# Kernel tuning notes

Hardware: AMD Instinct MI355X
Metric: run time of the kernel (lower is better)

The kernel has to match this reference:

```python
import jax, jax.numpy as jnp
import numpy as np

N = 500000      # num_edges
D = 128         # embedding_dim
S = 256         # num_samples (negatives)
TEMPERATURE = 0.1
EPS_NORM = 1e-12  # torch F.normalize eps
EPS_COS = 1e-8    # torch F.cosine_similarity eps


def setup_inputs() -> dict:
    key = jax.random.key(0)
    k1, k2, k3 = jax.random.split(key, 3)
    edge_embeddings = jax.random.normal(k1, (N, D), dtype=jnp.float32)
    positive_indices = jax.random.randint(k2, (N,), 0, N, dtype=jnp.int64)
    negative_indices = jax.random.randint(k3, (S,), 0, N, dtype=jnp.int64)
    return {
        "edge_embeddings": edge_embeddings,
        "positive_indices": positive_indices,
        "negative_indices": negative_indices,
    }


def _l2_normalize(x, eps):
    # matches torch: x / max(||x||_2, eps)
    n = jnp.sqrt(jnp.sum(x * x, axis=-1, keepdims=True))
    return x / jnp.maximum(n, eps)


def reference(edge_embeddings, positive_indices, negative_indices):
    # Normalize once; positives reuse the same per-row normalization.
    norm_all = _l2_normalize(edge_embeddings, EPS_NORM)          # [N, D]
    pos_norm = norm_all[positive_indices]                         # [N, D]
    positive_sim = jnp.sum(norm_all * pos_norm, axis=-1)          # [N]

    # cosine_similarity uses eps=1e-8 denominator clamp
    norm_all_cos = _l2_normalize(edge_embeddings, EPS_COS)        # [N, D]
    neg_norm = norm_all_cos[negative_indices]                     # [S, D]
    negative_sim = jnp.einsum('nd,sd->ns', norm_all_cos, neg_norm)  # [N, S]

    positive_logit = positive_sim / TEMPERATURE                   # [N]
    negative_logit = negative_sim / TEMPERATURE                   # [N, S]
    negative = jax.nn.logsumexp(negative_logit, axis=1) - jnp.log(jnp.float32(S))
    loss = -jnp.mean(positive_logit - negative)
    return loss
```

## Files before the change

kernel.cpp:

```cpp
#include <hip/hip_runtime.h>
#include <hip/hip_bf16.h>
#include <math.h>

#define D 128
#define S 256
#define ROWS 64
#define LOG_S 5.545177444479562f

typedef __attribute__((ext_vector_type(8)))  short    short8;
typedef __attribute__((ext_vector_type(8)))  __bf16   bf16x8;
typedef __attribute__((ext_vector_type(16))) float    floatx16;

typedef const __attribute__((address_space(1))) void gas_void;
typedef __attribute__((address_space(3))) void las_void;

__device__ __forceinline__ unsigned short f2bf(float x) {
  __hip_bfloat16 h = __float2bfloat16(x);
  return *(unsigned short*)&h;
}

__global__ void neg_norm_kernel(const float* __restrict__ emb,
                                const int* __restrict__ negidx,
                                unsigned short* __restrict__ negsw) {
  int s = blockIdx.x;
  int L = threadIdx.x;
  long idx = (long)negidx[s];
  float2 v = *(const float2*)(emb + idx * D + L * 2);
  float ss = v.x * v.x + v.y * v.y;
#pragma unroll
  for (int off = 1; off < 64; off <<= 1) ss += __shfl_xor(ss, off);
  float sc = 10.0f / fmaxf(sqrtf(ss), 1e-8f);
  int chunk = s >> 7, nr = s & 127;
  int lu = L >> 2, pos = (L & 3) * 2;
  int u = lu ^ (nr & 15);
  ushort2 o = make_ushort2(f2bf(v.x * sc), f2bf(v.y * sc));
  *(ushort2*)(negsw + chunk * 16384 + nr * 128 + u * 8 + pos) = o;
}

__global__ __launch_bounds__(256, 3)
void hyper_main(const float* __restrict__ emb,
                const int* __restrict__ posidx,
                const unsigned short* __restrict__ negsw,
                double* __restrict__ acc,
                int N) {
  __shared__ __align__(16) char smem[49152];
  unsigned short* rows_l = (unsigned short*)smem;
  unsigned short* negs_l = (unsigned short*)(smem + 16384);

  const int t = threadIdx.x;
  const int lane = t & 63;
  const int w = t >> 6;
  const long rbase = (long)blockIdx.x * ROWS;

  {
    const char* g = (const char*)negsw + w * 8192 + lane * 16;
    char* l = (char*)negs_l + w * 8192;
#pragma unroll
    for (int i = 0; i < 8; ++i)
      __builtin_amdgcn_global_load_lds((gas_void*)(g + i * 1024),
                                       (las_void*)(l + i * 1024), 16, 0, 0);
  }

  const int r  = t >> 2;
  const int qq = t & 3;
  long n = rbase + r;
  bool valid = (n < (long)N);
  long pi = 0;
  if (valid) pi = (long)posidx[n];

  float4 v[8];
  float ssv = 0.f, ssp = 0.f, dp = 0.f;
#pragma unroll
  for (int k = 0; k < 8; ++k) {
    int c4 = qq + 4 * k;
    float4 vv = make_float4(0.f, 0.f, 0.f, 0.f);
    float4 pp = make_float4(0.f, 0.f, 0.f, 0.f);
    if (valid) {
      vv = *(const float4*)(emb + n * D + c4 * 4);
      pp = *(const float4*)(emb + pi * D + c4 * 4);
    }
    v[k] = vv;
    ssv += vv.x*vv.x + vv.y*vv.y + vv.z*vv.z + vv.w*vv.w;
    ssp += pp.x*pp.x + pp.y*pp.y + pp.z*pp.z + pp.w*pp.w;
    dp  += vv.x*pp.x + vv.y*pp.y + vv.z*pp.z + vv.w*pp.w;
  }
#pragma unroll
  for (int off = 1; off < 4; off <<= 1) {
    ssv += __shfl_xor(ssv, off);
    ssp += __shfl_xor(ssp, off);
    dp  += __shfl_xor(dp,  off);
  }
  float inv8 = 1.0f / fmaxf(sqrtf(ssv), 1e-8f);
#pragma unroll
  for (int k = 0; k < 8; ++k) {
    int c4 = qq + 4 * k;
    int u = (c4 >> 1) ^ (r & 15);
    ushort4 o = make_ushort4(f2bf(v[k].x*inv8), f2bf(v[k].y*inv8),
                             f2bf(v[k].z*inv8), f2bf(v[k].w*inv8));
    *(ushort4*)&rows_l[r * 128 + u * 8 + (c4 & 1) * 4] = o;
  }
  float possum = 0.f;
  if (qq == 0 && valid) {
    float invv = 1.0f / fmaxf(sqrtf(ssv), 1e-12f);
    float invp = 1.0f / fmaxf(sqrtf(ssp), 1e-12f);
    possum = dp * invv * invp * 10.0f;
  }

  const int q   = lane >> 5;
  const int ln  = lane & 31;
  const int tr  = w >> 1;
  const int chh = w & 1;
  const int arow  = tr * 32 + ln;
  const int nrow0 = chh * 64 + ln;
  const int nrow1 = nrow0 + 32;

  float se[16];
#pragma unroll
  for (int i = 0; i < 16; ++i) se[i] = 0.f;

  for (int c = 0; c < 2; ++c) {
    __syncthreads();
    floatx16 acc0 = {};
    floatx16 acc1 = {};
#pragma unroll
    for (int ki = 0; ki < 8; ++ki) {
      int lu = ki * 2 + q;
      short8 a  = *(const short8*)&rows_l[arow  * 128 + (lu ^ (arow  & 15)) * 8];
      short8 b0 = *(const short8*)&negs_l[nrow0 * 128 + (lu ^ (nrow0 & 15)) * 8];
      short8 b1 = *(const short8*)&negs_l[nrow1 * 128 + (lu ^ (nrow1 & 15)) * 8];
      acc0 = __builtin_amdgcn_mfma_f32_32x32x16_bf16(
          __builtin_bit_cast(bf16x8, a), __builtin_bit_cast(bf16x8, b0), acc0, 0, 0, 0);
      acc1 = __builtin_amdgcn_mfma_f32_32x32x16_bf16(
          __builtin_bit_cast(bf16x8, a), __builtin_bit_cast(bf16x8, b1), acc1, 0, 0, 0);
    }
    if (c == 0) {
      __syncthreads();
      const char* g = (const char*)negsw + 32768 + w * 8192 + lane * 16;
      char* l = (char*)negs_l + w * 8192;
#pragma unroll
      for (int i = 0; i < 8; ++i)
        __builtin_amdgcn_global_load_lds((gas_void*)(g + i * 1024),
                                         (las_void*)(l + i * 1024), 16, 0, 0);
    }
#pragma unroll
    for (int rg = 0; rg < 16; ++rg)
      se[rg] += __expf(acc0[rg]) + __expf(acc1[rg]);
  }

#pragma unroll
  for (int rg = 0; rg < 16; ++rg) {
    float sv = se[rg];
#pragma unroll
    for (int off = 1; off < 32; off <<= 1) sv += __shfl_xor(sv, off);
    se[rg] = sv;
  }

  __syncthreads();
  float* sebuf = (float*)smem;
  if (ln == 0) {
#pragma unroll
    for (int rg = 0; rg < 16; ++rg) {
      int rr = tr * 32 + (rg & 3) + 8 * (rg >> 2) + 4 * q;
      sebuf[rr * 2 + chh] = se[rg];
    }
  }
  __syncthreads();

  float negterm = 0.f;
  if (t < 64) {
    long n2 = rbase + t;
    if (n2 < (long)N)
      negterm = __logf(sebuf[t * 2] + sebuf[t * 2 + 1]) - LOG_S;
  }

  float local = negterm - possum;
#pragma unroll
  for (int off = 1; off < 64; off <<= 1) local += __shfl_xor(local, off);
  float* red = (float*)(smem + 2048);
  if (lane == 0) red[w] = local;
  __syncthreads();
  if (t == 0) {
    double tot = (double)red[0] + (double)red[1] +
                 (double)red[2] + (double)red[3];
    atomicAdd(acc, tot);
  }
}

__global__ void finish_kernel(const double* __restrict__ acc,
                              float* __restrict__ out, int N) {
  out[0] = (float)(acc[0] / (double)N);
}

extern "C" void kernel_launch(void* const* d_in, const int* in_sizes, int n_in,
                              void* d_out, int out_size, void* d_ws, size_t ws_size,
                              hipStream_t stream) {
  const float* emb  = (const float*)d_in[0];
  const int* posidx = (const int*)d_in[1];
  const int* negidx = (const int*)d_in[2];
  int N = in_sizes[1];

  double* acc = (double*)d_ws;
  unsigned short* negsw = (unsigned short*)((char*)d_ws + 256);

  hipMemsetAsync(d_ws, 0, 256, stream);
  neg_norm_kernel<<<S, 64, 0, stream>>>(emb, negidx, negsw);
  int grid = (N + ROWS - 1) / ROWS;
  hyper_main<<<grid, 256, 0, stream>>>(emb, posidx, negsw, acc, N);
  finish_kernel<<<1, 1, 0, stream>>>(acc, (float*)d_out, N);
}
```

Before: 411.8 us.

## Keep A fragments in registers, double-buffer negative chunks, and use exp2 scaling

Each wave now owns 32 rows and converts its embeddings straight into MFMA A-fragments held in registers, with no round trip through LDS. The 256 negatives are streamed in four 64-row chunks through two LDS buffers so the next chunk loads while the current one is computed. Rows per block double to 128 and LDS drops to 32KB, allowing 4 blocks per CU. The logit scale folds in log2(e) so the exponential becomes a native exp2, and the cross-wave LDS reduction of per-row sums is removed. In exchange, register pressure rises from holding all A-fragments, and each row now runs more MFMA work per block.

```diff
diff --git a/kernel.cpp b/kernel.cpp
--- a/kernel.cpp
+++ b/kernel.cpp
@@ -4,8 +4,9 @@
 
 #define D 128
 #define S 256
-#define ROWS 64
+#define ROWS 128
 #define LOG_S 5.545177444479562f
+#define SCALE_EXP2 14.42695040888963f
 
 typedef __attribute__((ext_vector_type(8)))  short    short8;
 typedef __attribute__((ext_vector_type(8)))  __bf16   bf16x8;
@@ -14,9 +15,19 @@
 typedef const __attribute__((address_space(1))) void gas_void;
 typedef __attribute__((address_space(3))) void las_void;
 
+#if __has_builtin(__builtin_amdgcn_exp2f)
+#define EXP2(x) __builtin_amdgcn_exp2f(x)
+#else
+#define EXP2(x) exp2f(x)
+#endif
+
 __device__ __forceinline__ unsigned short f2bf(float x) {
   __hip_bfloat16 h = __float2bfloat16(x);
   return *(unsigned short*)&h;
+}
+
+__device__ __forceinline__ float dot4(float4 a, float4 b) {
+  return a.x*b.x + a.y*b.y + a.z*b.z + a.w*b.w;
 }
 
 __global__ void neg_norm_kernel(const float* __restrict__ emb,
@@ -29,122 +40,117 @@
   float ss = v.x * v.x + v.y * v.y;
 #pragma unroll
   for (int off = 1; off < 64; off <<= 1) ss += __shfl_xor(ss, off);
-  float sc = 10.0f / fmaxf(sqrtf(ss), 1e-8f);
-  int chunk = s >> 7, nr = s & 127;
+  float sc = SCALE_EXP2 / fmaxf(sqrtf(ss), 1e-8f);
+  int chunk = s >> 6, nr = s & 63;
   int lu = L >> 2, pos = (L & 3) * 2;
   int u = lu ^ (nr & 15);
   ushort2 o = make_ushort2(f2bf(v.x * sc), f2bf(v.y * sc));
-  *(ushort2*)(negsw + chunk * 16384 + nr * 128 + u * 8 + pos) = o;
-}
-
-__global__ __launch_bounds__(256, 3)
+  *(ushort2*)(negsw + chunk * 8192 + nr * 128 + u * 8 + pos) = o;
+}
+
+__global__ __launch_bounds__(256, 4)
 void hyper_main(const float* __restrict__ emb,
                 const int* __restrict__ posidx,
                 const unsigned short* __restrict__ negsw,
                 double* __restrict__ acc,
                 int N) {
-  __shared__ __align__(16) char smem[49152];
-  unsigned short* rows_l = (unsigned short*)smem;
-  unsigned short* negs_l = (unsigned short*)(smem + 16384);
+  __shared__ __align__(16) char smem[32768];
 
   const int t = threadIdx.x;
   const int lane = t & 63;
   const int w = t >> 6;
+  const int q = lane >> 5;
+  const int ln = lane & 31;
   const long rbase = (long)blockIdx.x * ROWS;
 
   {
-    const char* g = (const char*)negsw + w * 8192 + lane * 16;
-    char* l = (char*)negs_l + w * 8192;
-#pragma unroll
-    for (int i = 0; i < 8; ++i)
+    const char* g = (const char*)negsw + w * 4096 + lane * 16;
+    char* l = smem + w * 4096;
+#pragma unroll
+    for (int i = 0; i < 4; ++i)
       __builtin_amdgcn_global_load_lds((gas_void*)(g + i * 1024),
                                        (las_void*)(l + i * 1024), 16, 0, 0);
   }
 
-  const int r  = t >> 2;
-  const int qq = t & 3;
-  long n = rbase + r;
-  bool valid = (n < (long)N);
+  const long n = rbase + w * 32 + ln;
+  const bool valid = (n < (long)N);
   long pi = 0;
   if (valid) pi = (long)posidx[n];
 
-  float4 v[8];
+  float4 rv[8][2];
   float ssv = 0.f, ssp = 0.f, dp = 0.f;
 #pragma unroll
-  for (int k = 0; k < 8; ++k) {
-    int c4 = qq + 4 * k;
-    float4 vv = make_float4(0.f, 0.f, 0.f, 0.f);
-    float4 pp = make_float4(0.f, 0.f, 0.f, 0.f);
+  for (int ki = 0; ki < 8; ++ki) {
+    int off = (2 * ki + q) * 8;
+    float4 a0 = make_float4(0.f,0.f,0.f,0.f), a1 = a0, p0 = a0, p1 = a0;
     if (valid) {
-      vv = *(const float4*)(emb + n * D + c4 * 4);
-      pp = *(const float4*)(emb + pi * D + c4 * 4);
-    }
-    v[k] = vv;
-    ssv += vv.x*vv.x + vv.y*vv.y + vv.z*vv.z + vv.w*vv.w;
-    ssp += pp.x*pp.x + pp.y*pp.y + pp.z*pp.z + pp.w*pp.w;
-    dp  += vv.x*pp.x + vv.y*pp.y + vv.z*pp.z + vv.w*pp.w;
-  }
-#pragma unroll
-  for (int off = 1; off < 4; off <<= 1) {
-    ssv += __shfl_xor(ssv, off);
-    ssp += __shfl_xor(ssp, off);
-    dp  += __shfl_xor(dp,  off);
-  }
+      a0 = *(const float4*)(emb + n * D + off);
+      a1 = *(const float4*)(emb + n * D + off + 4);
+      p0 = *(const float4*)(emb + pi * D + off);
+      p1 = *(const float4*)(emb + pi * D + off + 4);
+    }
+    rv[ki][0] = a0; rv[ki][1] = a1;
+    ssv += dot4(a0, a0) + dot4(a1, a1);
+    ssp += dot4(p0, p0) + dot4(p1, p1);
+    dp  += dot4(a0, p0) + dot4(a1, p1);
+  }
+  ssv += __shfl_xor(ssv, 32);
+  ssp += __shfl_xor(ssp, 32);
+  dp  += __shfl_xor(dp,  32);
+
   float inv8 = 1.0f / fmaxf(sqrtf(ssv), 1e-8f);
-#pragma unroll
-  for (int k = 0; k < 8; ++k) {
-    int c4 = qq + 4 * k;
-    int u = (c4 >> 1) ^ (r & 15);
-    ushort4 o = make_ushort4(f2bf(v[k].x*inv8), f2bf(v[k].y*inv8),
-                             f2bf(v[k].z*inv8), f2bf(v[k].w*inv8));
-    *(ushort4*)&rows_l[r * 128 + u * 8 + (c4 & 1) * 4] = o;
-  }
+  short8 afrag[8];
+#pragma unroll
+  for (int ki = 0; ki < 8; ++ki) {
+    float4 a0 = rv[ki][0], a1 = rv[ki][1];
+    short8 t8;
+    t8[0] = (short)f2bf(a0.x * inv8); t8[1] = (short)f2bf(a0.y * inv8);
+    t8[2] = (short)f2bf(a0.z * inv8); t8[3] = (short)f2bf(a0.w * inv8);
+    t8[4] = (short)f2bf(a1.x * inv8); t8[5] = (short)f2bf(a1.y * inv8);
+    t8[6] = (short)f2bf(a1.z * inv8); t8[7] = (short)f2bf(a1.w * inv8);
+    afrag[ki] = t8;
+  }
+
   float possum = 0.f;
-  if (qq == 0 && valid) {
+  if (q == 0 && valid) {
     float invv = 1.0f / fmaxf(sqrtf(ssv), 1e-12f);
     float invp = 1.0f / fmaxf(sqrtf(ssp), 1e-12f);
     possum = dp * invv * invp * 10.0f;
   }
 
-  const int q   = lane >> 5;
-  const int ln  = lane & 31;
-  const int tr  = w >> 1;
-  const int chh = w & 1;
-  const int arow  = tr * 32 + ln;
-  const int nrow0 = chh * 64 + ln;
-  const int nrow1 = nrow0 + 32;
-
   float se[16];
 #pragma unroll
   for (int i = 0; i < 16; ++i) se[i] = 0.f;
 
-  for (int c = 0; c < 2; ++c) {
+  const int ulocal = (ln & 15);
+  for (int c = 0; c < 4; ++c) {
     __syncthreads();
+    if (c < 3) {
+      const char* g = (const char*)negsw + (c + 1) * 16384 + w * 4096 + lane * 16;
+      char* l = smem + ((c + 1) & 1) * 16384 + w * 4096;
+#pragma unroll
+      for (int i = 0; i < 4; ++i)
+        __builtin_amdgcn_global_load_lds((gas_void*)(g + i * 1024),
+                                         (las_void*)(l + i * 1024), 16, 0, 0);
+    }
+    const unsigned short* buf = (const unsigned short*)(smem + (c & 1) * 16384);
+
     floatx16 acc0 = {};
     floatx16 acc1 = {};
 #pragma unroll
     for (int ki = 0; ki < 8; ++ki) {
-      int lu = ki * 2 + q;
-      short8 a  = *(const short8*)&rows_l[arow  * 128 + (lu ^ (arow  & 15)) * 8];
-      short8 b0 = *(const short8*)&negs_l[nrow0 * 128 + (lu ^ (nrow0 & 15)) * 8];
-      short8 b1 = *(const short8*)&negs_l[nrow1 * 128 + (lu ^ (nrow1 & 15)) * 8];
+      int lu = 2 * ki + q;
+      int u8 = (lu ^ ulocal) * 8;
+      short8 b0 = *(const short8*)&buf[ln * 128 + u8];
+      short8 b1 = *(const short8*)&buf[(ln + 32) * 128 + u8];
       acc0 = __builtin_amdgcn_mfma_f32_32x32x16_bf16(
-          __builtin_bit_cast(bf16x8, a), __builtin_bit_cast(bf16x8, b0), acc0, 0, 0, 0);
+          __builtin_bit_cast(bf16x8, afrag[ki]), __builtin_bit_cast(bf16x8, b0), acc0, 0, 0, 0);
       acc1 = __builtin_amdgcn_mfma_f32_32x32x16_bf16(
-          __builtin_bit_cast(bf16x8, a), __builtin_bit_cast(bf16x8, b1), acc1, 0, 0, 0);
-    }
-    if (c == 0) {
-      __syncthreads();
-      const char* g = (const char*)negsw + 32768 + w * 8192 + lane * 16;
-      char* l = (char*)negs_l + w * 8192;
-#pragma unroll
-      for (int i = 0; i < 8; ++i)
-        __builtin_amdgcn_global_load_lds((gas_void*)(g + i * 1024),
-                                         (las_void*)(l + i * 1024), 16, 0, 0);
+          __builtin_bit_cast(bf16x8, afrag[ki]), __builtin_bit_cast(bf16x8, b1), acc1, 0, 0, 0);
     }
 #pragma unroll
     for (int rg = 0; rg < 16; ++rg)
-      se[rg] += __expf(acc0[rg]) + __expf(acc1[rg]);
+      se[rg] += EXP2(acc0[rg]) + EXP2(acc1[rg]);
   }
 
 #pragma unroll
@@ -155,28 +161,20 @@
     se[rg] = sv;
   }
 
-  __syncthreads();
-  float* sebuf = (float*)smem;
+  float negsum = 0.f;
   if (ln == 0) {
 #pragma unroll
     for (int rg = 0; rg < 16; ++rg) {
-      int rr = tr * 32 + (rg & 3) + 8 * (rg >> 2) + 4 * q;
-      sebuf[rr * 2 + chh] = se[rg];
-    }
-  }
-  __syncthreads();
-
-  float negterm = 0.f;
-  if (t < 64) {
-    long n2 = rbase + t;
-    if (n2 < (long)N)
-      negterm = __logf(sebuf[t * 2] + sebuf[t * 2 + 1]) - LOG_S;
-  }
-
-  float local = negterm - possum;
+      int rr = w * 32 + (rg & 3) + 8 * (rg >> 2) + 4 * q;
+      long n2 = rbase + rr;
+      if (n2 < (long)N) negsum += __logf(se[rg]) - LOG_S;
+    }
+  }
+
+  float local = negsum - possum;
 #pragma unroll
   for (int off = 1; off < 64; off <<= 1) local += __shfl_xor(local, off);
-  float* red = (float*)(smem + 2048);
+  float* red = (float*)smem;
   if (lane == 0) red[w] = local;
   __syncthreads();
   if (t == 0) {
```

Measured after the change: 532.6 us. 29.3% more time.
